# Kernel optimization log

Measured on AMD Instinct MI355X. Metric: run time of the kernel, lower is better.

## Reference

```python
import jax, jax.numpy as jnp
import numpy as np


def setup_inputs() -> dict:
    key = jax.random.key(0)
    k1, k2, k3 = jax.random.split(key, 3)
    B, C, H, W = 32, 128, 64, 64
    z = jax.random.normal(k1, (B, C, H, W, 2), dtype=jnp.float32)
    gamma = jnp.eye(2, dtype=jnp.float32) / jnp.sqrt(jnp.float32(2.0)) \
        + 0.01 * jax.random.normal(k2, (2, 2), dtype=jnp.float32)
    beta = 0.01 * jax.random.normal(k3, (2,), dtype=jnp.float32)
    return {"z": z, "gamma": gamma, "beta": beta}


def reference(z, gamma, beta):
    # z: [B, C, H, W, 2] real view of complex input. Training-mode C_BatchNorm.
    B, C, H, W, _ = z.shape
    N = C * H * W
    zf = z.reshape(B, N, 2)
    mu = jnp.mean(zf, axis=0)                 # [N, 2]
    xc = zf - mu                              # [B, N, 2]
    # Per-position 2x2 covariance over batch (unbiased, /(B-1)).
    sigma = jnp.einsum('bni,bnj->nij', xc, xc) / jnp.asarray(B - 1, zf.dtype)  # [N,2,2]
    # Closed-form 2x2 "inverse-sqrt" as written in the source: (M + s*I)/t.
    trace = sigma[:, 0, 0] + sigma[:, 1, 1]
    det = sigma[:, 0, 0] * sigma[:, 1, 1] - sigma[:, 0, 1] * sigma[:, 1, 0]
    s = jnp.sqrt(det)
    t = jnp.sqrt(trace + 2.0 * s)
    eye2 = jnp.eye(2, dtype=zf.dtype)
    m_inv = (sigma + s[:, None, None] * eye2) / t[:, None, None]  # [N,2,2]
    # Whitening (per-position 2x2 matvec) + affine gamma/beta.
    o = jnp.einsum('nij,bnj->bni', m_inv, xc)                     # [B,N,2]
    o = jnp.einsum('ij,bnj->bni', gamma, o) + beta                # [B,N,2]
    return o.reshape(B, C, H, W, 2)
```

## Files before the change

kernel.cpp:

```cpp
#include <hip/hip_runtime.h>


constexpr int BATCH = 32;

typedef float f32x2 __attribute__((ext_vector_type(2)));

__global__ __launch_bounds__(256) void cbn_kernel(
    const float2* __restrict__ z,
    const float* __restrict__ gamma,
    const float* __restrict__ beta,
    float2* __restrict__ out,
    int N)
{
    int n = blockIdx.x * blockDim.x + threadIdx.x;
    if (n >= N) return;

    float2 v[BATCH];
#pragma unroll
    for (int b = 0; b < BATCH; ++b) {
        v[b] = z[(size_t)b * N + n];
    }
#pragma unroll
    for (int b = 0; b < BATCH; ++b) {
        asm volatile("" : "+v"(v[b].x), "+v"(v[b].y));
    }

    float sx = 0.f, sy = 0.f, sxx = 0.f, sxy = 0.f, syy = 0.f;
#pragma unroll
    for (int b = 0; b < BATCH; ++b) {
        float2 q = v[b];
        sx += q.x; sy += q.y;
        sxx = fmaf(q.x, q.x, sxx);
        sxy = fmaf(q.x, q.y, sxy);
        syy = fmaf(q.y, q.y, syy);
    }

    const float invB  = 1.0f / BATCH;
    const float invB1 = 1.0f / (BATCH - 1);

    float mx = sx * invB, my = sy * invB;
    float cxx = (sxx - BATCH * mx * mx) * invB1;
    float cxy = (sxy - BATCH * mx * my) * invB1;
    float cyy = (syy - BATCH * my * my) * invB1;

    float s  = sqrtf(cxx * cyy - cxy * cxy);
    float rt = 1.0f / sqrtf(cxx + cyy + 2.0f * s);
    float a00 = (cxx + s) * rt;
    float a01 = cxy * rt;
    float a11 = (cyy + s) * rt;

    const float g00 = gamma[0], g01 = gamma[1], g10 = gamma[2], g11 = gamma[3];
    const float be0 = beta[0], be1 = beta[1];

    float c00 = g00 * a00 + g01 * a01;
    float c01 = g00 * a01 + g01 * a11;
    float c10 = g10 * a00 + g11 * a01;
    float c11 = g10 * a01 + g11 * a11;

#pragma unroll
    for (int b = 0; b < BATCH; ++b) {
        float dx = v[b].x - mx;
        float dy = v[b].y - my;
        f32x2 o;
        o.x = fmaf(c00, dx, fmaf(c01, dy, be0));
        o.y = fmaf(c10, dx, fmaf(c11, dy, be1));
        __builtin_nontemporal_store(o, (f32x2*)&out[(size_t)b * N + n]);
    }
}

extern "C" void kernel_launch(void* const* d_in, const int* in_sizes, int n_in,
                              void* d_out, int out_size, void* d_ws, size_t ws_size,
                              hipStream_t stream) {
    const float2* z    = (const float2*)d_in[0];
    const float* gamma = (const float*)d_in[1];
    const float* beta  = (const float*)d_in[2];
    float2* out = (float2*)d_out;

    int N = in_sizes[0] / (BATCH * 2);

    dim3 block(256);
    dim3 grid((N + block.x - 1) / block.x);
    hipLaunchKernelGGL(cbn_kernel, grid, block, 0, stream, z, gamma, beta, out, N);
}
```

Baseline: 49.71 us.

## Split batchnorm into a stats kernel and a float4 apply kernel

Replaces the single fused kernel with two passes. The first computes per-position mean and covariance and writes the folded affine matrix and offset to workspace. The second re-reads z as float4 and spreads the batch across more threads (8 batches per thread) to apply the transform. The aim is higher occupancy and wider memory accesses than holding 32 batch values per thread, at the cost of reading z a second time plus an extra workspace round trip. The apply kernel also hardcodes a shift of 18 bits, so it only works for this input shape.

```diff
diff --git a/kernel.cpp b/kernel.cpp
--- a/kernel.cpp
+++ b/kernel.cpp
@@ -3,32 +3,23 @@
 
 constexpr int BATCH = 32;
 
-typedef float f32x2 __attribute__((ext_vector_type(2)));
+typedef float f32x4 __attribute__((ext_vector_type(4)));
 
-__global__ __launch_bounds__(256) void cbn_kernel(
+__global__ __launch_bounds__(256) void cbn_stats(
     const float2* __restrict__ z,
     const float* __restrict__ gamma,
     const float* __restrict__ beta,
-    float2* __restrict__ out,
+    float4* __restrict__ cmat,
+    float2* __restrict__ coff,
     int N)
 {
     int n = blockIdx.x * blockDim.x + threadIdx.x;
     if (n >= N) return;
 
-    float2 v[BATCH];
-#pragma unroll
-    for (int b = 0; b < BATCH; ++b) {
-        v[b] = z[(size_t)b * N + n];
-    }
-#pragma unroll
-    for (int b = 0; b < BATCH; ++b) {
-        asm volatile("" : "+v"(v[b].x), "+v"(v[b].y));
-    }
-
     float sx = 0.f, sy = 0.f, sxx = 0.f, sxy = 0.f, syy = 0.f;
 #pragma unroll
     for (int b = 0; b < BATCH; ++b) {
-        float2 q = v[b];
+        float2 q = z[(size_t)b * N + n];
         sx += q.x; sy += q.y;
         sxx = fmaf(q.x, q.x, sxx);
         sxy = fmaf(q.x, q.y, sxy);
@@ -57,10 +48,86 @@
     float c10 = g10 * a00 + g11 * a01;
     float c11 = g10 * a01 + g11 * a11;
 
+    float d0 = be0 - c00 * mx - c01 * my;
+    float d1 = be1 - c10 * mx - c11 * my;
+
+    cmat[n] = make_float4(c00, c10, c01, c11);
+    coff[n] = make_float2(d0, d1);
+}
+
+__global__ __launch_bounds__(256) void cbn_apply(
+    const float4* __restrict__ z4,
+    const float4* __restrict__ cmat,
+    const float4* __restrict__ coff4,
+    float4* __restrict__ out4,
+    int N2)
+{
+    int t = blockIdx.x * blockDim.x + threadIdx.x;
+    int g = t >> 18;
+    int c = t & (N2 - 1);
+
+    float4 m0 = cmat[2 * c];
+    float4 m1 = cmat[2 * c + 1];
+    float4 d  = coff4[c];
+
+#pragma unroll
+    for (int k = 0; k < 8; ++k) {
+        int b = g * 8 + k;
+        float4 q = z4[(size_t)b * N2 + c];
+        f32x4 o;
+        o.x = fmaf(m0.x, q.x, fmaf(m0.z, q.y, d.x));
+        o.y = fmaf(m0.y, q.x, fmaf(m0.w, q.y, d.y));
+        o.z = fmaf(m1.x, q.z, fmaf(m1.z, q.w, d.z));
+        o.w = fmaf(m1.y, q.z, fmaf(m1.w, q.w, d.w));
+        __builtin_nontemporal_store(o, (f32x4*)&out4[(size_t)b * N2 + c]);
+    }
+}
+
+typedef float f32x2 __attribute__((ext_vector_type(2)));
+
+__global__ __launch_bounds__(256) void cbn_fallback(
+    const float2* __restrict__ z,
+    const float* __restrict__ gamma,
+    const float* __restrict__ beta,
+    float2* __restrict__ out,
+    int N)
+{
+    int n = blockIdx.x * blockDim.x + threadIdx.x;
+    if (n >= N) return;
+
+    float2 v[BATCH];
+#pragma unroll
+    for (int b = 0; b < BATCH; ++b) v[b] = z[(size_t)b * N + n];
+#pragma unroll
+    for (int b = 0; b < BATCH; ++b)
+        asm volatile("" : "+v"(v[b].x), "+v"(v[b].y));
+
+    float sx = 0.f, sy = 0.f, sxx = 0.f, sxy = 0.f, syy = 0.f;
 #pragma unroll
     for (int b = 0; b < BATCH; ++b) {
-        float dx = v[b].x - mx;
-        float dy = v[b].y - my;
+        float2 q = v[b];
+        sx += q.x; sy += q.y;
+        sxx = fmaf(q.x, q.x, sxx);
+        sxy = fmaf(q.x, q.y, sxy);
+        syy = fmaf(q.y, q.y, syy);
+    }
+    const float invB = 1.0f / BATCH, invB1 = 1.0f / (BATCH - 1);
+    float mx = sx * invB, my = sy * invB;
+    float cxx = (sxx - BATCH * mx * mx) * invB1;
+    float cxy = (sxy - BATCH * mx * my) * invB1;
+    float cyy = (syy - BATCH * my * my) * invB1;
+    float s  = sqrtf(cxx * cyy - cxy * cxy);
+    float rt = 1.0f / sqrtf(cxx + cyy + 2.0f * s);
+    float a00 = (cxx + s) * rt, a01 = cxy * rt, a11 = (cyy + s) * rt;
+    const float g00 = gamma[0], g01 = gamma[1], g10 = gamma[2], g11 = gamma[3];
+    const float be0 = beta[0], be1 = beta[1];
+    float c00 = g00 * a00 + g01 * a01;
+    float c01 = g00 * a01 + g01 * a11;
+    float c10 = g10 * a00 + g11 * a01;
+    float c11 = g10 * a01 + g11 * a11;
+#pragma unroll
+    for (int b = 0; b < BATCH; ++b) {
+        float dx = v[b].x - mx, dy = v[b].y - my;
         f32x2 o;
         o.x = fmaf(c00, dx, fmaf(c01, dy, be0));
         o.y = fmaf(c10, dx, fmaf(c11, dy, be1));
@@ -71,14 +138,32 @@
 extern "C" void kernel_launch(void* const* d_in, const int* in_sizes, int n_in,
                               void* d_out, int out_size, void* d_ws, size_t ws_size,
                               hipStream_t stream) {
-    const float2* z    = (const float2*)d_in[0];
+    const float* z     = (const float*)d_in[0];
     const float* gamma = (const float*)d_in[1];
     const float* beta  = (const float*)d_in[2];
-    float2* out = (float2*)d_out;
 
-    int N = in_sizes[0] / (BATCH * 2);
+    int N  = in_sizes[0] / (BATCH * 2);
+    int N2 = N / 2;
 
-    dim3 block(256);
-    dim3 grid((N + block.x - 1) / block.x);
-    hipLaunchKernelGGL(cbn_kernel, grid, block, 0, stream, z, gamma, beta, out, N);
+    size_t need = (size_t)N * 16 + (size_t)N * 8;
+
+    if (ws_size >= need && (N2 & (N2 - 1)) == 0) {
+        float4* cmat = (float4*)d_ws;
+        float2* coff = (float2*)((char*)d_ws + (size_t)N * 16);
+
+        dim3 block(256);
+        dim3 grid1((N + 255) / 256);
+        hipLaunchKernelGGL(cbn_stats, grid1, block, 0, stream,
+                           (const float2*)z, gamma, beta, cmat, coff, N);
+
+        dim3 grid2((unsigned)(((size_t)N2 * 4) / 256));
+        hipLaunchKernelGGL(cbn_apply, grid2, block, 0, stream,
+                           (const float4*)z, (const float4*)cmat,
+                           (const float4*)coff, (float4*)d_out, N2);
+    } else {
+        dim3 block(256);
+        dim3 grid((N + 255) / 256);
+        hipLaunchKernelGGL(cbn_fallback, grid, block, 0, stream,
+                           (const float2*)z, gamma, beta, (float2*)d_out, N);
+    }
 }
```

Result: slower. 80.96 us (+62.8%).
